# Performance work log

Measured on AMD Instinct MI355X. Metric: run time of the kernel, lower is better.

Reference implementation:

```python
import jax, jax.numpy as jnp
import numpy as np

B, S, HID = 1, 2048, 2048
H, KVH, D = 16, 8, 128
QR, KR, VR = 6, 2, 2
SOFTCAP = 50.0
SCALING = D ** -0.5
NEG = -1e9


def _rope(Bfac, cos, sin):
    # Bfac: [b, s, r, d]; cos/sin: [s, d//2]; rotates adjacent pairs (complex view)
    x = Bfac.reshape(*Bfac.shape[:-1], D // 2, 2)
    xe, xo = x[..., 0], x[..., 1]
    c = cos[None, :, None, :]
    s = sin[None, :, None, :]
    oe = xe * c - xo * s
    oo = xe * s + xo * c
    return jnp.stack([oe, oo], axis=-1).reshape(Bfac.shape)


def setup_inputs() -> dict:
    key = jax.random.key(0)
    ks = jax.random.split(key, 12)
    hidden_states = jax.random.normal(ks[0], (B, S, HID), jnp.float32)
    # rotary tables (standard RoPE frequencies)
    inv_freq = 1.0 / (10000.0 ** (jnp.arange(0, D, 2, dtype=jnp.float32) / D))
    t = jnp.arange(S, dtype=jnp.float32)
    ang = t[:, None] * inv_freq[None, :]            # [S, D//2]
    cos, sin = jnp.cos(ang), jnp.sin(ang)
    # causal additive mask [1,1,S,S]
    causal = jnp.tril(jnp.ones((S, S), bool))
    mask = jnp.where(causal, 0.0, NEG).astype(jnp.float32)[None, None]
    kv_write_indices = jnp.arange(S, dtype=jnp.int32)
    sc = lambda k, shp: jax.random.normal(k, shp, jnp.float32) * (shp[0] ** -0.5)
    return {
        "hidden_states": hidden_states, "cos": cos, "sin": sin, "mask": mask,
        "kv_write_indices": kv_write_indices,
        "WAq": sc(ks[1], (HID, H * QR)), "WAk": sc(ks[2], (HID, KVH * KR)),
        "WAv": sc(ks[3], (HID, KVH * VR)), "WBq": sc(ks[4], (HID, QR * D)),
        "WBk": sc(ks[5], (HID, KR * D)), "WBv": sc(ks[6], (HID, VR * D)),
        "Wo": sc(ks[7], (H * D, HID)),
    }


def reference(hidden_states, cos, sin, mask, kv_write_indices,
              WAq, WAk, WAv, WBq, WBk, WBv, Wo):
    b, s, _ = hidden_states.shape
    # factor projections (never materialize full Q/K/V)
    A_q = (hidden_states @ WAq).reshape(b, s, H, QR)
    A_k = (hidden_states @ WAk).reshape(b, s, KVH, KR)
    A_v = (hidden_states @ WAv).reshape(b, s, KVH, VR)
    B_q = (hidden_states @ WBq).reshape(b, s, QR, D)
    B_k = (hidden_states @ WBk).reshape(b, s, KR, D)
    B_v = (hidden_states @ WBv).reshape(b, s, VR, D)
    # RoPE on B factors
    B_q = _rope(B_q, cos, sin)
    B_k = _rope(B_k, cos, sin)
    # prefill: kv_write_indices = arange(S) => cache slices equal current factors
    # GQA: broadcast KV heads up to H
    hpk = H // KVH
    A_k = jnp.repeat(A_k, hpk, axis=2)   # [b,k,H,KR]
    A_v = jnp.repeat(A_v, hpk, axis=2)   # [b,k,H,VR]
    # factor-expanded attention scores
    B_dots = jnp.einsum('bqrd,bksd->bqkrs', B_q, B_k) * SCALING
    attn = jnp.einsum('bqhr,bkhs,bqkrs->bhqk', A_q, A_k, B_dots)
    # logit softcapping
    attn = SOFTCAP * jnp.tanh(attn / SOFTCAP)
    attn = attn + mask
    probs = jax.nn.softmax(attn.astype(jnp.float32), axis=-1).astype(hidden_states.dtype)
    # factor-expanded output
    out = jnp.einsum('bhqk,bkhu,bkud->bhqd', probs, A_v, B_v)
    out = out.transpose(0, 2, 1, 3).reshape(b, s, H * D)
    return out @ Wo
```

## Files before the change

kernel.cpp:

```cpp
#include <hip/hip_runtime.h>


constexpr int SEQ   = 2048;
constexpr int HIDN  = 2048;
constexpr int NHEAD = 16;
constexpr int NKVH  = 8;
constexpr int DH    = 128;
constexpr int NCOLS = 1408;

typedef __bf16 bf16x8 __attribute__((ext_vector_type(8)));
typedef float  f32x4  __attribute__((ext_vector_type(4)));

#define MFMA(a, b, c) __builtin_amdgcn_mfma_f32_16x16x32_bf16((a), (b), (c), 0, 0, 0)

__device__ __forceinline__ void gload_lds16(const void* g, void* l) {
  __builtin_amdgcn_global_load_lds(
      (const __attribute__((address_space(1))) void*)g,
      (__attribute__((address_space(3))) void*)l, 16, 0, 0);
}


__global__ __launch_bounds__(256) void k_prep(
    const float* __restrict__ hidden,
    const float* __restrict__ WAq, const float* __restrict__ WAk,
    const float* __restrict__ WAv, const float* __restrict__ WBq,
    const float* __restrict__ WBk, const float* __restrict__ WBv,
    const float* __restrict__ Wo,
    __bf16* __restrict__ hid_bf, __bf16* __restrict__ WT,
    __bf16* __restrict__ WoT) {
  const int bid = blockIdx.x;
  if (bid < 2048) {
    const int i = (bid * 256 + threadIdx.x) * 8;
    f32x4 a = *(const f32x4*)(hidden + i);
    f32x4 b = *(const f32x4*)(hidden + i + 4);
    bf16x8 v;
#pragma unroll
    for (int j = 0; j < 4; j++) { v[j] = (__bf16)a[j]; v[4 + j] = (__bf16)b[j]; }
    *(bf16x8*)(hid_bf + i) = v;
  } else if (bid < 2048 + 44 * 64) {
    const int t = bid - 2048;
    const int bc = (t % 44) * 32, bk = (t / 44) * 32;
    __shared__ float tl[32][33];
    const int tx = threadIdx.x & 31, ty = threadIdx.x >> 5;
    const int c = bc + tx;
#pragma unroll
    for (int j = 0; j < 32; j += 8) {
      const int k = bk + ty + j;
      float v;
      if (c < 96)        v = WAq[k * 96 + c];
      else if (c < 112)  v = WAk[k * 16 + (c - 96)];
      else if (c < 128)  v = WAv[k * 16 + (c - 112)];
      else if (c < 896)  v = WBq[k * 768 + (c - 128)];
      else if (c < 1152) v = WBk[k * 256 + (c - 896)];
      else               v = WBv[k * 256 + (c - 1152)];
      tl[ty + j][tx] = v;
    }
    __syncthreads();
#pragma unroll
    for (int j = 0; j < 32; j += 8)
      WT[(size_t)(bc + ty + j) * HIDN + bk + tx] = (__bf16)tl[tx][ty + j];
  } else {
    const int t = bid - (2048 + 44 * 64);
    const int bn = (t % 64) * 32, bk = (t / 64) * 32;
    __shared__ float tl[32][33];
    const int tx = threadIdx.x & 31, ty = threadIdx.x >> 5;
#pragma unroll
    for (int j = 0; j < 32; j += 8)
      tl[ty + j][tx] = Wo[(size_t)(bk + ty + j) * HIDN + bn + tx];
    __syncthreads();
#pragma unroll
    for (int j = 0; j < 32; j += 8)
      WoT[(size_t)(bn + ty + j) * HIDN + bk + tx] = (__bf16)tl[tx][ty + j];
  }
}


__global__ __launch_bounds__(256) void k_gemm_bt(const __bf16* __restrict__ A,
                                                 const __bf16* __restrict__ BT,
                                                 float* __restrict__ C,
                                                 int M, int N, int K) {
  __shared__ __bf16 As[4][4096];
  __shared__ __bf16 Bs[4][2048];
  const int tid = threadIdx.x;
  const int w = tid >> 6, lane = tid & 63;
  const int lhi = lane >> 4, llo = lane & 15;
  const int wr = w >> 1, wc = w & 1;

  const int nx = gridDim.x, ny = gridDim.y;
  const int id = blockIdx.y * nx + blockIdx.x;
  int brow, bcol;
  if (((ny & 1) == 0) && ((nx & 3) == 0)) {
    const int g = id & 7, k = id >> 3;
    const int rows = ny >> 1, cols = nx >> 2;
    const int rg = g >> 2, cg = g & 3;
    const int r = k % rows, c = k / rows;
    brow = (rg * rows + r) * 128;
    bcol = (cg * cols + c) * 64;
  } else {
    const int cpx = (nx * ny) >> 3;
    const int sid = (id & 7) * cpx + (id >> 3);
    brow = (sid / nx) * 128;
    bcol = (sid % nx) * 64;
  }

  const int rA = lane >> 2, kA = (lane & 3) * 8;
  const int nt = K >> 5;

  f32x4 acc[4][2];
#pragma unroll
  for (int m = 0; m < 4; m++)
#pragma unroll
    for (int n = 0; n < 2; n++) acc[m][n] = (f32x4){0.f, 0.f, 0.f, 0.f};

  auto stage = [&](int t) {
    const int buf = t & 3;
    const int k0 = t * 32;
#pragma unroll
    for (int i = 0; i < 2; i++) {
      int seg = w * 2 + i;
      int row = seg * 16 + rA;
      gload_lds16(A + (size_t)(brow + row) * K + k0 + kA, &As[buf][seg * 512]);
    }
    gload_lds16(BT + (size_t)(bcol + w * 16 + rA) * K + k0 + kA, &Bs[buf][w * 512]);
  };

  stage(0); stage(1); stage(2);
  asm volatile("s_waitcnt vmcnt(6)" ::: "memory");
  __builtin_amdgcn_s_barrier();

  for (int t = 0; t < nt; t++) {
    if (t + 3 < nt) stage(t + 3);
    const int buf = t & 3;
    bf16x8 af[4], bfr[2];
#pragma unroll
    for (int m = 0; m < 4; m++)
      af[m] = *(const bf16x8*)&As[buf][(wr * 64 + m * 16 + llo) * 32 + lhi * 8];
#pragma unroll
    for (int n = 0; n < 2; n++)
      bfr[n] = *(const bf16x8*)&Bs[buf][(wc * 32 + n * 16 + llo) * 32 + lhi * 8];
#pragma unroll
    for (int m = 0; m < 4; m++)
#pragma unroll
      for (int n = 0; n < 2; n++) acc[m][n] = MFMA(af[m], bfr[n], acc[m][n]);
    const int rem = nt - 2 - t;
    if (rem >= 2)      asm volatile("s_waitcnt vmcnt(6)" ::: "memory");
    else if (rem == 1) asm volatile("s_waitcnt vmcnt(3)" ::: "memory");
    else               asm volatile("s_waitcnt vmcnt(0)" ::: "memory");
    __builtin_amdgcn_s_barrier();
  }

#pragma unroll
  for (int m = 0; m < 4; m++)
#pragma unroll
    for (int n = 0; n < 2; n++) {
      int r0 = brow + wr * 64 + m * 16 + lhi * 4;
      int c0 = bcol + wc * 32 + n * 16 + llo;
#pragma unroll
      for (int r = 0; r < 4; r++) C[(size_t)(r0 + r) * N + c0] = acc[m][n][r];
    }
}


__global__ __launch_bounds__(128) void k_build_qkv(const float* __restrict__ P,
                                                   const float* __restrict__ cosT,
                                                   const float* __restrict__ sinT,
                                                   __bf16* __restrict__ Qo,
                                                   __bf16* __restrict__ Ko,
                                                   __bf16* __restrict__ Vto) {
  const int q = blockIdx.x, d = threadIdx.x;
  __shared__ float Ash[128];
  const float* row = P + (size_t)q * NCOLS;
  Ash[d] = row[d];
  __syncthreads();
  const int m2 = (d >> 1) * 2;
  const bool odd = d & 1;
  const float c = cosT[q * 64 + (d >> 1)];
  const float s = sinT[q * 64 + (d >> 1)];

  float qacc[16];
#pragma unroll
  for (int h = 0; h < 16; h++) qacc[h] = 0.f;
#pragma unroll
  for (int r = 0; r < 6; r++) {
    float xe = row[128 + r * 128 + m2];
    float xo = row[128 + r * 128 + m2 + 1];
    float br = odd ? (xe * s + xo * c) : (xe * c - xo * s);
#pragma unroll
    for (int h = 0; h < 16; h++) qacc[h] += Ash[h * 6 + r] * br;
  }
#pragma unroll
  for (int h = 0; h < 16; h++)
    Qo[((size_t)h * SEQ + q) * DH + d] = (__bf16)(qacc[h] * 0.08838834764831845f);

  float kacc[8];
#pragma unroll
  for (int g = 0; g < 8; g++) kacc[g] = 0.f;
#pragma unroll
  for (int ss = 0; ss < 2; ss++) {
    float xe = row[896 + ss * 128 + m2];
    float xo = row[896 + ss * 128 + m2 + 1];
    float bs = odd ? (xe * s + xo * c) : (xe * c - xo * s);
#pragma unroll
    for (int g = 0; g < 8; g++) kacc[g] += Ash[96 + g * 2 + ss] * bs;
  }
#pragma unroll
  for (int g = 0; g < 8; g++)
    Ko[((size_t)g * SEQ + q) * DH + d] = (__bf16)kacc[g];

  float vacc[8];
#pragma unroll
  for (int g = 0; g < 8; g++) vacc[g] = 0.f;
#pragma unroll
  for (int u = 0; u < 2; u++) {
    float vu = row[1152 + u * 128 + d];
#pragma unroll
    for (int g = 0; g < 8; g++) vacc[g] += Ash[112 + g * 2 + u] * vu;
  }
#pragma unroll
  for (int g = 0; g < 8; g++)
    Vto[((size_t)g * DH + d) * SEQ + q] = (__bf16)vacc[g];
}


__global__ __launch_bounds__(256) void k_attn(const __bf16* __restrict__ Q,
                                              const __bf16* __restrict__ Kc,
                                              const __bf16* __restrict__ Vt,
                                              float* __restrict__ AOf0,
                                              float* __restrict__ AOf1,
                                              float* __restrict__ Ls) {
  const int raw = blockIdx.x;
  const int g = raw & 7;
  const int j = raw >> 3;
  const int bqi = 31 - (j >> 2);
  const int hh = (j >> 1) & 1;
  const int p = j & 1;
  const int h = g * 2 + hh;
  const int w = threadIdx.x >> 6, lane = threadIdx.x & 63;
  const int lhi = lane >> 4, llo = lane & 15;
  const int q0 = bqi * 64 + w * 16;
  const int t0 = p * (bqi + 1), t1 = t0 + bqi + 1;

  __shared__ __bf16 KVs[2][8192];

  const __bf16* Qh = Q  + (size_t)h * SEQ * DH;
  const __bf16* Kg = Kc + (size_t)g * SEQ * DH;
  const __bf16* Vg = Vt + (size_t)g * DH * SEQ;
  float* AOc = p ? AOf1 : AOf0;

  bf16x8 aq[4];
#pragma unroll
  for (int c = 0; c < 4; c++)
    aq[c] = *(const bf16x8*)&Qh[(size_t)(q0 + llo) * DH + c * 32 + lhi * 8];

  f32x4 oacc[8];
  float lsum = 0.f;
#pragma unroll
  for (int n = 0; n < 8; n++) oacc[n] = (f32x4){0.f, 0.f, 0.f, 0.f};

  const int swv = (llo >> 1) & 3;
  const int vb0 = ((((lhi >> 1) ^ swv) << 4) | ((lhi & 1) << 3)) + llo * 64;
  const int vb1 = (((((lhi >> 1) + 2) ^ swv) << 4) | ((lhi & 1) << 3)) + llo * 64;

  auto stage = [&](int kb, int buf) {
    __bf16* L = KVs[buf];
    if (w < 2) {
#pragma unroll
      for (int u = 0; u < 4; u++) {
        int c = w * 256 + u * 64 + lane;
        int row = c >> 4, jj = c & 15;
        gload_lds16(Kg + (size_t)(kb + row) * DH + ((jj ^ (row & 7)) * 8),
                    L + (w * 256 + u * 64) * 8);
      }
    } else {
#pragma unroll
      for (int u = 0; u < 4; u++) {
        int c = (w - 2) * 256 + u * 64 + lane;
        int d = c >> 2, jj = c & 3;
        gload_lds16(Vg + (size_t)d * SEQ + kb + ((jj ^ ((d >> 1) & 3)) * 8),
                    L + 4096 + ((w - 2) * 256 + u * 64) * 8);
      }
    }
  };

  stage(t0 * 32, t0 & 1);
  for (int t = t0; t < t1; t++) {
    const int kb = t * 32;
    const int buf = t & 1;
    if (t + 1 < t1) {
      stage(kb + 32, buf ^ 1);
      asm volatile("s_waitcnt vmcnt(4)" ::: "memory");
    } else {
      asm volatile("s_waitcnt vmcnt(0)" ::: "memory");
    }
    __builtin_amdgcn_s_barrier();
    if (kb <= q0 + 15) {
      const char* Kl = (const char*)KVs[buf];
      const char* Vl = (const char*)(KVs[buf] + 4096);
      f32x4 s0 = {0.f, 0.f, 0.f, 0.f}, s1 = {0.f, 0.f, 0.f, 0.f};
#pragma unroll
      for (int c = 0; c < 4; c++) {
        const int row0 = llo, row1 = 16 + llo;
        bf16x8 k0 = *(const bf16x8*)(Kl + row0 * 256 +
                                     ((c * 64 + lhi * 16) ^ ((row0 & 7) << 4)));
        bf16x8 k1 = *(const bf16x8*)(Kl + row1 * 256 +
                                     ((c * 64 + lhi * 16) ^ ((row1 & 7) << 4)));
        s0 = MFMA(k0, aq[c], s0);
        s1 = MFMA(k1, aq[c], s1);
      }
      float e[8];
#pragma unroll
      for (int r = 0; r < 4; r++) {
        float a0 = exp2f(s0[r] * 0.057707802f);
        float a1 = exp2f(s1[r] * 0.057707802f);
        e[r]     = exp2f(72.134752f - 144.269504f * __builtin_amdgcn_rcpf(a0 + 1.f));
        e[4 + r] = exp2f(72.134752f - 144.269504f * __builtin_amdgcn_rcpf(a1 + 1.f));
      }
      if (kb + 31 > q0) {
        const int qrow = q0 + llo;
#pragma unroll
        for (int r = 0; r < 4; r++) {
          if (kb + lhi * 4 + r > qrow)      e[r] = 0.f;
          if (kb + 16 + lhi * 4 + r > qrow) e[4 + r] = 0.f;
        }
      }
#pragma unroll
      for (int r = 0; r < 4; r++) lsum += e[r] + e[4 + r];
      union { bf16x8 v8; unsigned u[4]; } pu;
      asm("v_cvt_pk_bf16_f32 %0, %1, %2" : "=v"(pu.u[0]) : "v"(e[0]), "v"(e[1]));
      asm("v_cvt_pk_bf16_f32 %0, %1, %2" : "=v"(pu.u[1]) : "v"(e[2]), "v"(e[3]));
      asm("v_cvt_pk_bf16_f32 %0, %1, %2" : "=v"(pu.u[2]) : "v"(e[4]), "v"(e[5]));
      asm("v_cvt_pk_bf16_f32 %0, %1, %2" : "=v"(pu.u[3]) : "v"(e[6]), "v"(e[7]));
#pragma unroll
      for (int n = 0; n < 8; n++) {
        union { bf16x8 v8; struct { uint2 lo, hi; } d; } vu;
        vu.d.lo = *(const uint2*)(Vl + vb0 + n * 1024);
        vu.d.hi = *(const uint2*)(Vl + vb1 + n * 1024);
        oacc[n] = MFMA(pu.v8, vu.v8, oacc[n]);
      }
    }
    asm volatile("" ::: "memory");
    __builtin_amdgcn_s_barrier();
  }

  float tsum = lsum;
  tsum += __shfl_xor(tsum, 16);
  tsum += __shfl_xor(tsum, 32);
  if (lhi == 0) Ls[((size_t)p * NHEAD + h) * SEQ + q0 + llo] = tsum;
#pragma unroll
  for (int r = 0; r < 4; r++) {
    const int qrow = q0 + lhi * 4 + r;
#pragma unroll
    for (int n = 0; n < 8; n++)
      AOc[(size_t)qrow * HIDN + h * DH + n * 16 + llo] = oacc[n][r];
  }
}


__global__ __launch_bounds__(256) void k_norm(const float* __restrict__ A0,
                                              const float* __restrict__ A1,
                                              const float* __restrict__ Ls,
                                              __bf16* __restrict__ AO) {
  const int i = (blockIdx.x * 256 + threadIdx.x) * 4;
  const int q = i >> 11, h = (i & 2047) >> 7;
  const float inv = 1.f / (Ls[h * SEQ + q] + Ls[(NHEAD + h) * SEQ + q]);
  f32x4 a = *(const f32x4*)(A0 + i);
  f32x4 b = *(const f32x4*)(A1 + i);
#pragma unroll
  for (int j = 0; j < 4; j++) AO[i + j] = (__bf16)((a[j] + b[j]) * inv);
}


extern "C" void kernel_launch(void* const* d_in, const int* in_sizes, int n_in,
                              void* d_out, int out_size, void* d_ws, size_t ws_size,
                              hipStream_t stream) {
  const float* hidden = (const float*)d_in[0];
  const float* cosT   = (const float*)d_in[1];
  const float* sinT   = (const float*)d_in[2];
  const float* WAq = (const float*)d_in[5];
  const float* WAk = (const float*)d_in[6];
  const float* WAv = (const float*)d_in[7];
  const float* WBq = (const float*)d_in[8];
  const float* WBk = (const float*)d_in[9];
  const float* WBv = (const float*)d_in[10];
  const float* Wo  = (const float*)d_in[11];
  float* out = (float*)d_out;

  char* ws = (char*)d_ws;
  __bf16* hid_bf = (__bf16*)(ws);
  __bf16* WallT  = (__bf16*)(ws + 8388608);
  float*  Pproj  = (float*)(ws + 14155776);
  __bf16* WoT    = (__bf16*)(ws + 25690112);
  __bf16* Qb     = (__bf16*)(ws + 34078720);
  __bf16* Kb     = (__bf16*)(ws + 42467328);
  __bf16* Vt     = (__bf16*)(ws + 46661632);
  float*  AOf0   = (float*)(ws);
  float*  AOf1   = (float*)(ws + 50855936);
  float*  Ls     = (float*)(ws + 67633152);
  __bf16* AO     = (__bf16*)(ws + 34078720);

  k_prep<<<2048 + 44 * 64 + 64 * 64, 256, 0, stream>>>(
      hidden, WAq, WAk, WAv, WBq, WBk, WBv, Wo, hid_bf, WallT, WoT);
  k_gemm_bt<<<dim3(NCOLS / 64, SEQ / 128), 256, 0, stream>>>(hid_bf, WallT, Pproj,
                                                             SEQ, NCOLS, HIDN);
  k_build_qkv<<<SEQ, 128, 0, stream>>>(Pproj, cosT, sinT, Qb, Kb, Vt);
  k_attn<<<1024, 256, 0, stream>>>(Qb, Kb, Vt, AOf0, AOf1, Ls);
  k_norm<<<(SEQ * HIDN / 4) / 256, 256, 0, stream>>>(AOf0, AOf1, Ls, AO);
  k_gemm_bt<<<dim3(HIDN / 64, SEQ / 128), 256, 0, stream>>>(AO, WoT, out,
                                                            SEQ, HIDN, HIDN);
}
```

Baseline: 161.6 us.

## Overlap Wo transpose with projection GEMM and widen output GEMM tiles

```diff
diff --git a/kernel.cpp b/kernel.cpp
--- a/kernel.cpp
+++ b/kernel.cpp
@@ -25,9 +25,7 @@
     const float* __restrict__ WAq, const float* __restrict__ WAk,
     const float* __restrict__ WAv, const float* __restrict__ WBq,
     const float* __restrict__ WBk, const float* __restrict__ WBv,
-    const float* __restrict__ Wo,
-    __bf16* __restrict__ hid_bf, __bf16* __restrict__ WT,
-    __bf16* __restrict__ WoT) {
+    __bf16* __restrict__ hid_bf, __bf16* __restrict__ WT) {
   const int bid = blockIdx.x;
   if (bid < 2048) {
     const int i = (bid * 256 + threadIdx.x) * 8;
@@ -37,7 +35,7 @@
 #pragma unroll
     for (int j = 0; j < 4; j++) { v[j] = (__bf16)a[j]; v[4 + j] = (__bf16)b[j]; }
     *(bf16x8*)(hid_bf + i) = v;
-  } else if (bid < 2048 + 44 * 64) {
+  } else {
     const int t = bid - 2048;
     const int bc = (t % 44) * 32, bk = (t / 44) * 32;
     __shared__ float tl[32][33];
@@ -59,10 +57,20 @@
 #pragma unroll
     for (int j = 0; j < 32; j += 8)
       WT[(size_t)(bc + ty + j) * HIDN + bk + tx] = (__bf16)tl[tx][ty + j];
-  } else {
-    const int t = bid - (2048 + 44 * 64);
+  }
+}
+
+
+__global__ __launch_bounds__(256) void k_proj_wo(
+    const __bf16* __restrict__ A, const __bf16* __restrict__ BT,
+    float* __restrict__ C, const float* __restrict__ Wo,
+    __bf16* __restrict__ WoT) {
+  __shared__ char smem[49152];
+  const int bid = blockIdx.x;
+  if (bid >= 352) {
+    const int t = bid - 352;
     const int bn = (t % 64) * 32, bk = (t / 64) * 32;
-    __shared__ float tl[32][33];
+    float (*tl)[33] = (float(*)[33])smem;
     const int tx = threadIdx.x & 31, ty = threadIdx.x >> 5;
 #pragma unroll
     for (int j = 0; j < 32; j += 8)
@@ -71,38 +79,17 @@
 #pragma unroll
     for (int j = 0; j < 32; j += 8)
       WoT[(size_t)(bn + ty + j) * HIDN + bk + tx] = (__bf16)tl[tx][ty + j];
-  }
-}
-
-
-__global__ __launch_bounds__(256) void k_gemm_bt(const __bf16* __restrict__ A,
-                                                 const __bf16* __restrict__ BT,
-                                                 float* __restrict__ C,
-                                                 int M, int N, int K) {
-  __shared__ __bf16 As[4][4096];
-  __shared__ __bf16 Bs[4][2048];
+    return;
+  }
+  const int K = HIDN, N = NCOLS;
+  __bf16* As = (__bf16*)smem;
+  __bf16* Bs = (__bf16*)(smem + 32768);
   const int tid = threadIdx.x;
   const int w = tid >> 6, lane = tid & 63;
   const int lhi = lane >> 4, llo = lane & 15;
   const int wr = w >> 1, wc = w & 1;
-
-  const int nx = gridDim.x, ny = gridDim.y;
-  const int id = blockIdx.y * nx + blockIdx.x;
-  int brow, bcol;
-  if (((ny & 1) == 0) && ((nx & 3) == 0)) {
-    const int g = id & 7, k = id >> 3;
-    const int rows = ny >> 1, cols = nx >> 2;
-    const int rg = g >> 2, cg = g & 3;
-    const int r = k % rows, c = k / rows;
-    brow = (rg * rows + r) * 128;
-    bcol = (cg * cols + c) * 64;
-  } else {
-    const int cpx = (nx * ny) >> 3;
-    const int sid = (id & 7) * cpx + (id >> 3);
-    brow = (sid / nx) * 128;
-    bcol = (sid % nx) * 64;
-  }
-
+  const int sid = (bid & 7) * 44 + (bid >> 3);
+  const int brow = (sid / 22) * 128, bcol = (sid % 22) * 64;
   const int rA = lane >> 2, kA = (lane & 3) * 8;
   const int nt = K >> 5;
 
@@ -119,9 +106,11 @@
     for (int i = 0; i < 2; i++) {
       int seg = w * 2 + i;
       int row = seg * 16 + rA;
-      gload_lds16(A + (size_t)(brow + row) * K + k0 + kA, &As[buf][seg * 512]);
-    }
-    gload_lds16(BT + (size_t)(bcol + w * 16 + rA) * K + k0 + kA, &Bs[buf][w * 512]);
+      gload_lds16(A + (size_t)(brow + row) * K + k0 + kA,
+                  As + buf * 4096 + seg * 512);
+    }
+    gload_lds16(BT + (size_t)(bcol + w * 16 + rA) * K + k0 + kA,
+                Bs + buf * 2048 + w * 512);
   };
 
   stage(0); stage(1); stage(2);
@@ -134,10 +123,10 @@
     bf16x8 af[4], bfr[2];
 #pragma unroll
     for (int m = 0; m < 4; m++)
-      af[m] = *(const bf16x8*)&As[buf][(wr * 64 + m * 16 + llo) * 32 + lhi * 8];
+      af[m] = *(const bf16x8*)&As[buf * 4096 + (wr * 64 + m * 16 + llo) * 32 + lhi * 8];
 #pragma unroll
     for (int n = 0; n < 2; n++)
-      bfr[n] = *(const bf16x8*)&Bs[buf][(wc * 32 + n * 16 + llo) * 32 + lhi * 8];
+      bfr[n] = *(const bf16x8*)&Bs[buf * 2048 + (wc * 32 + n * 16 + llo) * 32 + lhi * 8];
 #pragma unroll
     for (int m = 0; m < 4; m++)
 #pragma unroll
@@ -145,6 +134,76 @@
     const int rem = nt - 2 - t;
     if (rem >= 2)      asm volatile("s_waitcnt vmcnt(6)" ::: "memory");
     else if (rem == 1) asm volatile("s_waitcnt vmcnt(3)" ::: "memory");
+    else               asm volatile("s_waitcnt vmcnt(0)" ::: "memory");
+    __builtin_amdgcn_s_barrier();
+  }
+
+#pragma unroll
+  for (int m = 0; m < 4; m++)
+#pragma unroll
+    for (int n = 0; n < 2; n++) {
+      int r0 = brow + wr * 64 + m * 16 + lhi * 4;
+      int c0 = bcol + wc * 32 + n * 16 + llo;
+#pragma unroll
+      for (int r = 0; r < 4; r++) C[(size_t)(r0 + r) * N + c0] = acc[m][n][r];
+    }
+}
+
+
+__global__ __launch_bounds__(512) void k_gemm_out(const __bf16* __restrict__ A,
+                                                  const __bf16* __restrict__ BT,
+                                                  float* __restrict__ C) {
+  __shared__ __bf16 As[4][4096];
+  __shared__ __bf16 Bs[4][4096];
+  const int K = HIDN, N = HIDN;
+  const int tid = threadIdx.x;
+  const int w = tid >> 6, lane = tid & 63;
+  const int lhi = lane >> 4, llo = lane & 15;
+  const int wr = w >> 2, wc = w & 3;
+
+  const int id = blockIdx.y * 16 + blockIdx.x;
+  const int g = id & 7, kk = id >> 3;
+  const int rg = g >> 2, cg = g & 3;
+  const int brow = (rg * 8 + (kk & 7)) * 128;
+  const int bcol = (cg * 4 + (kk >> 3)) * 128;
+
+  const int rA = tid >> 2, kA = (tid & 3) * 8;
+  const int nt = K >> 5;
+
+  f32x4 acc[4][2];
+#pragma unroll
+  for (int m = 0; m < 4; m++)
+#pragma unroll
+    for (int n = 0; n < 2; n++) acc[m][n] = (f32x4){0.f, 0.f, 0.f, 0.f};
+
+  auto stage = [&](int t) {
+    const int buf = t & 3;
+    const int k0 = t * 32;
+    gload_lds16(A  + (size_t)(brow + rA) * K + k0 + kA, &As[buf][w * 512]);
+    gload_lds16(BT + (size_t)(bcol + rA) * K + k0 + kA, &Bs[buf][w * 512]);
+  };
+
+  stage(0); stage(1); stage(2);
+  asm volatile("s_waitcnt vmcnt(4)" ::: "memory");
+  __builtin_amdgcn_s_barrier();
+
+  for (int t = 0; t < nt; t++) {
+    if (t + 3 < nt) stage(t + 3);
+    const int buf = t & 3;
+    bf16x8 af[4], bfr[2];
+#pragma unroll
+    for (int m = 0; m < 4; m++)
+      af[m] = *(const bf16x8*)&As[buf][(wr * 64 + m * 16 + llo) * 32 + lhi * 8];
+#pragma unroll
+    for (int n = 0; n < 2; n++)
+      bfr[n] = *(const bf16x8*)&Bs[buf][(wc * 32 + n * 16 + llo) * 32 + lhi * 8];
+#pragma unroll
+    for (int m = 0; m < 4; m++)
+#pragma unroll
+      for (int n = 0; n < 2; n++) acc[m][n] = MFMA(af[m], bfr[n], acc[m][n]);
+    const int rem = nt - 2 - t;
+    if (rem >= 2)      asm volatile("s_waitcnt vmcnt(4)" ::: "memory");
+    else if (rem == 1) asm volatile("s_waitcnt vmcnt(2)" ::: "memory");
     else               asm volatile("s_waitcnt vmcnt(0)" ::: "memory");
     __builtin_amdgcn_s_barrier();
   }
@@ -398,13 +457,11 @@
   float*  Ls     = (float*)(ws + 67633152);
   __bf16* AO     = (__bf16*)(ws + 34078720);
 
-  k_prep<<<2048 + 44 * 64 + 64 * 64, 256, 0, stream>>>(
-      hidden, WAq, WAk, WAv, WBq, WBk, WBv, Wo, hid_bf, WallT, WoT);
-  k_gemm_bt<<<dim3(NCOLS / 64, SEQ / 128), 256, 0, stream>>>(hid_bf, WallT, Pproj,
-                                                             SEQ, NCOLS, HIDN);
+  k_prep<<<2048 + 44 * 64, 256, 0, stream>>>(
+      hidden, WAq, WAk, WAv, WBq, WBk, WBv, hid_bf, WallT);
+  k_proj_wo<<<352 + 4096, 256, 0, stream>>>(hid_bf, WallT, Pproj, Wo, WoT);
   k_build_qkv<<<SEQ, 128, 0, stream>>>(Pproj, cosT, sinT, Qb, Kb, Vt);
   k_attn<<<1024, 256, 0, stream>>>(Qb, Kb, Vt, AOf0, AOf1, Ls);
   k_norm<<<(SEQ * HIDN / 4) / 256, 256, 0, stream>>>(AOf0, AOf1, Ls, AO);
-  k_gemm_bt<<<dim3(HIDN / 64, SEQ / 128), 256, 0, stream>>>(AO, WoT, out,
-                                                            SEQ, HIDN, HIDN);
-}
+  k_gemm_out<<<dim3(16, 16), 512, 0, stream>>>(AO, WoT, out);
+}
```

Measured after the change: 153.7 us. -4.9%, faster.
